# Performance work log

Hardware: AMD Instinct MI355X
Metric: run time of the kernel (lower is better)

Reference implementation:

```python
import jax, jax.numpy as jnp
import numpy as np
import math

B, L, D, H = 8, 2048, 1024, 1024


def setup_inputs() -> dict:
    key = jax.random.key(0)
    ks = jax.random.split(key, 6)
    scale = 1.0 / math.sqrt(D)
    return {
        "input_q": jax.random.normal(ks[0], (B, L, D), dtype=jnp.float32),
        "input_k": jax.random.normal(ks[1], (B, L, D), dtype=jnp.float32),
        "k_mask": jax.random.uniform(ks[2], (B, L), dtype=jnp.float32),
        "Wq": jax.random.normal(ks[3], (D, H), dtype=jnp.float32) * scale,
        "bq": jnp.zeros((H,), dtype=jnp.float32),
        "Wk": jax.random.normal(ks[4], (D, H), dtype=jnp.float32) * scale,
        "bk": jnp.zeros((H,), dtype=jnp.float32),
    }


def reference(input_q, input_k, k_mask, Wq, bq, Wk, bk):
    # Linear projections: (b, l, d) @ (d, h) -> (b, l, h)
    q = input_q @ Wq + bq
    k = input_k @ Wk + bk
    # Faithful to original: mask values become 0.0 or -1e9, then an
    # outer product bmm((b,l,1),(b,1,l)) builds the (b,l,l) additive mask.
    m = jnp.where(k_mask > 0.5, 0.0, -1000000000.0)  # (b, l)
    add_mask = m[:, :, None] * m[:, None, :]          # (b, l, l) outer product
    # Scaled dot-product scores
    attn = jnp.einsum("bqh,bkh->bqk", q, k) / math.sqrt(H)
    attn = jax.nn.softmax(attn + add_mask, axis=-1)
    # Weighted sum over the ORIGINAL input_k (not projected k), as in source
    out = jnp.einsum("bqk,bkd->bqd", attn, input_k)
    return out
```

## Files before the change

### kernel.cpp

```cpp
#include <hip/hip_runtime.h>

#define BATCH 8
#define SEQ   2048
#define DIM   1024

typedef __attribute__((ext_vector_type(8)))  short short8;
typedef __attribute__((ext_vector_type(4)))  short short4v;
typedef __attribute__((ext_vector_type(4)))  float floatx4;
typedef __attribute__((ext_vector_type(16))) float floatx16;

__device__ __forceinline__ unsigned short f32_to_bf16(float f) {
    union { float f; unsigned int u; } x; x.f = f;
    unsigned int r = x.u + 0x7fffu + ((x.u >> 16) & 1u);
    return (unsigned short)(r >> 16);
}

__device__ __forceinline__ float bf16_to_f32(unsigned short h) {
    union { unsigned int u; float f; } x; x.u = ((unsigned int)h) << 16;
    return x.f;
}

__device__ __forceinline__ void async_load16(const void* g, void* l) {
    __builtin_amdgcn_global_load_lds(
        (const __attribute__((address_space(1))) void*)g,
        (__attribute__((address_space(3))) void*)l, 16, 0, 0);
}

__global__ __launch_bounds__(256) void build_idx(
    const float* __restrict__ mask, int* __restrict__ idx,
    int* __restrict__ cnt, int* __restrict__ padcnt)
{
    const int b = blockIdx.x;
    const int t = threadIdx.x;
    const float* mb = mask + b * SEQ;
    int flags[8]; int c = 0;
#pragma unroll
    for (int j = 0; j < 8; ++j) {
        flags[j] = (mb[t * 8 + j] > 0.5f) ? 1 : 0;
        c += flags[j];
    }
    int sc = c;
    for (int o = 1; o < 64; o <<= 1) {
        int v = __shfl_up(sc, o);
        if ((t & 63) >= o) sc += v;
    }
    __shared__ int wtot[4];
    const int lane = t & 63, wave = t >> 6;
    if (lane == 63) wtot[wave] = sc;
    __syncthreads();
    int woff = 0;
    for (int w = 0; w < wave; ++w) woff += wtot[w];
    int p = woff + sc - c;
#pragma unroll
    for (int j = 0; j < 8; ++j)
        if (flags[j]) idx[b * SEQ + (p++)] = t * 8 + j;
    __syncthreads();
    const int total = wtot[0] + wtot[1] + wtot[2] + wtot[3];
    if (t == 0) { cnt[b] = total; padcnt[b] = (total + 127) & ~127; }
    for (int q = total + t; q < SEQ; q += 256) idx[b * SEQ + q] = 0;
}

__global__ __launch_bounds__(256) void gather_cvt_q(
    const float* __restrict__ xq, const int* __restrict__ idx,
    const int* __restrict__ padcnt, unsigned short* __restrict__ qc)
{
    const int b = blockIdx.y;
    const int rc = blockIdx.x;
    if (rc >= padcnt[b]) return;
    const int src = idx[b * SEQ + rc];
    const float* s = xq + ((long)b * SEQ + src) * DIM + threadIdx.x * 4;
    unsigned short* d = qc + ((long)b * SEQ + rc) * DIM + threadIdx.x * 4;
    floatx4 v = *(const floatx4*)s;
    short4v w;
#pragma unroll
    for (int j = 0; j < 4; ++j) w[j] = (short)f32_to_bf16(v[j]);
    *(short4v*)d = w;
}

__global__ __launch_bounds__(256) void prep_kv(
    const float* __restrict__ xk, const float* __restrict__ mask,
    unsigned short* __restrict__ kbf, unsigned short* __restrict__ Vt,
    float* __restrict__ mavg)
{
    __shared__ float tile[32][33];
    __shared__ float msk[32];
    __shared__ float csum[8][32];
    const int b  = blockIdx.z;
    const int c0 = blockIdx.x * 32;
    const int r0 = blockIdx.y * 32;
    const int tx = threadIdx.x & 31, ty = threadIdx.x >> 5;
    const float* xb = xk + (long)b * SEQ * DIM;
    unsigned short* kb = kbf + (long)b * SEQ * DIM;
    unsigned short* vb = Vt + (long)b * DIM * SEQ;

    if (threadIdx.x < 32) msk[threadIdx.x] = mask[b * SEQ + r0 + threadIdx.x];

    float v[4];
#pragma unroll
    for (int i = 0; i < 4; ++i) {
        const int r = ty + i * 8;
        v[i] = xb[(long)(r0 + r) * DIM + c0 + tx];
        tile[r][tx] = v[i];
        kb[(long)(r0 + r) * DIM + c0 + tx] = f32_to_bf16(v[i]);
    }
    __syncthreads();

    float s = 0.f;
#pragma unroll
    for (int i = 0; i < 4; ++i) {
        const int r = ty + i * 8;
        s += (msk[r] <= 0.5f) ? v[i] : 0.f;
    }
    csum[ty][tx] = s;

#pragma unroll
    for (int i = 0; i < 4; ++i) {
        const int c = ty + i * 8;
        vb[(long)(c0 + c) * SEQ + r0 + tx] = f32_to_bf16(tile[tx][c]);
    }
    __syncthreads();
    if (ty == 0) {
        float t = 0.f;
#pragma unroll
        for (int j = 0; j < 8; ++j) t += csum[j][tx];
        atomicAdd(&mavg[b * DIM + c0 + tx], t);
    }
}

__global__ __launch_bounds__(256) void cvt_bf16_2(
    const float* __restrict__ s0, unsigned short* __restrict__ d0,
    const float* __restrict__ s1, unsigned short* __restrict__ d1)
{
    const int hi = blockIdx.x >> 9;
    const float* src = hi ? s1 : s0;
    unsigned short* dst = hi ? d1 : d0;
    const long i = ((long)(blockIdx.x & 511) * 256 + threadIdx.x) * 8;
    floatx4 v0 = *(const floatx4*)(src + i);
    floatx4 v1 = *(const floatx4*)(src + i + 4);
    short8 w;
#pragma unroll
    for (int j = 0; j < 4; ++j) w[j]     = (short)f32_to_bf16(v0[j]);
#pragma unroll
    for (int j = 0; j < 4; ++j) w[4 + j] = (short)f32_to_bf16(v1[j]);
    *(short8*)(dst + i) = w;
}

__global__ __launch_bounds__(256) void proj_bias(
    const float* __restrict__ bq, const float* __restrict__ Wk, float* __restrict__ g0)
{
    const int n = blockIdx.x;
    const int t = threadIdx.x;
    float s = 0.f;
    for (int h = t; h < DIM; h += 256) s += bq[h] * Wk[(long)n * DIM + h];
    for (int o = 32; o; o >>= 1) s += __shfl_xor(s, o);
    __shared__ float r[4];
    if ((t & 63) == 0) r[t >> 6] = s;
    __syncthreads();
    if (t == 0) g0[n] = r[0] + r[1] + r[2] + r[3];
}

template<bool C_BF16, bool BIAS, bool LIMIT, bool SCATTER, int FLAT>
__global__ __launch_bounds__(256, 4) void gemm_bt(
    const unsigned short* __restrict__ A, const unsigned short* __restrict__ Bt,
    void* __restrict__ Cp, const float* __restrict__ bias,
    int N, int K, long sA, long sB, long sC, float scale,
    const int* __restrict__ mlim, const int* __restrict__ cntp,
    const int* __restrict__ idx, int sh)
{
    int bx, by, bz;
    if (FLAT == 0) {
        bx = blockIdx.x; by = blockIdx.y; bz = blockIdx.z;
    } else {
        const int id = blockIdx.x;
        bz = id & 7;
        const int rem = id >> 3;
        const int m = (1 << sh) - 1;
        if (FLAT == 1) { bx = rem & m; by = rem >> sh; }
        else           { by = rem & m; bx = rem >> sh; }
    }
    const int row0 = bx * 128;
    if (LIMIT && row0 >= mlim[bz]) return;

    __shared__ unsigned short As[128 * 64];
    __shared__ unsigned short Bs[128 * 64];

    const int tid  = threadIdx.x;
    const int lane = tid & 63;
    const int wave = tid >> 6;
    const int wm   = wave >> 1;
    const int wn   = wave & 1;
    const int l31  = lane & 31;
    const int half = lane >> 5;
    const int x7   = lane & 7;
    const int col0 = by * 128;

    const int sr = lane >> 3;
    const int sq = ((lane & 7) ^ sr) * 8;

    const long K8 = (long)K * 8;
    const unsigned short* aRow =
        A + (long)bz * sA + (long)row0 * K + (long)(wave * 32 + sr) * K + sq;
    const unsigned short* bRow =
        Bt + (long)bz * sB + (long)col0 * K + (long)(wave * 32 + sr) * K + sq;

    floatx16 acc[2][2];
#pragma unroll
    for (int a = 0; a < 2; ++a)
#pragma unroll
        for (int b = 0; b < 2; ++b)
#pragma unroll
            for (int r = 0; r < 16; ++r) acc[a][b][r] = 0.f;

    const int raf[2] = { (wm * 64 +  0 + l31) * 64, (wm * 64 + 32 + l31) * 64 };
    const int rbf[2] = { (wn * 64 +  0 + l31) * 64, (wn * 64 + 32 + l31) * 64 };

    for (int kt = 0; kt < K; kt += 64) {
#pragma unroll
        for (int c = 0; c < 4; ++c) {
            const int chunk = wave * 4 + c;
            async_load16(aRow + kt + c * K8, As + chunk * 512);
            async_load16(bRow + kt + c * K8, Bs + chunk * 512);
        }
        __syncthreads();

#pragma unroll
        for (int ks = 0; ks < 4; ++ks) {
            const int sw = ((ks * 2 + half) ^ x7) << 3;
            short8 af[2], bf[2];
#pragma unroll
            for (int t = 0; t < 2; ++t) {
                af[t] = *(const short8*)(As + raf[t] + sw);
                bf[t] = *(const short8*)(Bs + rbf[t] + sw);
            }
#pragma unroll
            for (int tm = 0; tm < 2; ++tm)
#pragma unroll
                for (int tn = 0; tn < 2; ++tn)
                    acc[tm][tn] = __builtin_amdgcn_mfma_f32_32x32x16_bf16(
                        af[tm], bf[tn], acc[tm][tn], 0, 0, 0);
        }
        __syncthreads();
    }

    const long zC = (long)bz * sC;
    const int climit = SCATTER ? cntp[bz] : 0;
    const int* ridx  = SCATTER ? (idx + bz * SEQ) : (const int*)nullptr;
#pragma unroll
    for (int tn = 0; tn < 2; ++tn) {
        const int ccol = col0 + wn * 64 + tn * 32 + l31;
        float bv = 0.f;
        if (BIAS) bv = bias[ccol];
#pragma unroll
        for (int tm = 0; tm < 2; ++tm) {
            const int rbase = row0 + wm * 64 + tm * 32 + 4 * half;
#pragma unroll
            for (int r = 0; r < 16; ++r) {
                const int crow = rbase + (r & 3) + 8 * (r >> 2);
                float v = acc[tm][tn][r] * scale + bv;
                long orow = crow;
                if (SCATTER) {
                    if (crow >= climit) continue;
                    orow = ridx[crow];
                }
                const long ci = zC + orow * (long)N + ccol;
                if (C_BF16) ((unsigned short*)Cp)[ci] = f32_to_bf16(v);
                else        ((float*)Cp)[ci] = v;
            }
        }
    }
}

__global__ __launch_bounds__(256) void softmax_rows(
    unsigned short* __restrict__ S, const int* __restrict__ padcnt)
{
    const int b = blockIdx.x >> 11, rc = blockIdx.x & 2047;
    if (rc >= padcnt[b]) return;
    const long base = (long)blockIdx.x * SEQ + threadIdx.x * 8;
    const int lane = threadIdx.x & 63, wave = threadIdx.x >> 6;
    __shared__ float rbuf[8];

    short8 v = *(const short8*)(S + base);
    float x[8];
#pragma unroll
    for (int j = 0; j < 8; ++j) x[j] = bf16_to_f32((unsigned short)v[j]);

    float m = x[0];
#pragma unroll
    for (int j = 1; j < 8; ++j) m = fmaxf(m, x[j]);
    for (int o = 32; o; o >>= 1) m = fmaxf(m, __shfl_xor(m, o));
    if (lane == 0) rbuf[wave] = m;
    __syncthreads();
    m = fmaxf(fmaxf(rbuf[0], rbuf[1]), fmaxf(rbuf[2], rbuf[3]));

    float e[8], s = 0.f;
#pragma unroll
    for (int j = 0; j < 8; ++j) { e[j] = __expf(x[j] - m); s += e[j]; }
    for (int o = 32; o; o >>= 1) s += __shfl_xor(s, o);
    if (lane == 0) rbuf[4 + wave] = s;
    __syncthreads();
    s = rbuf[4] + rbuf[5] + rbuf[6] + rbuf[7];
    const float inv = 1.0f / s;

    short8 o8;
#pragma unroll
    for (int j = 0; j < 8; ++j) o8[j] = (short)f32_to_bf16(e[j] * inv);
    *(short8*)(S + base) = o8;
}

__global__ __launch_bounds__(256) void overwrite_masked(
    float* __restrict__ out, const float* __restrict__ mask,
    const float* __restrict__ mavg, const int* __restrict__ cnt)
{
    const int bid = blockIdx.x;
    const int b = bid >> 11;
    if (mask[bid] > 0.5f) return;
    const float inv = 1.0f / (float)(SEQ - cnt[b]);
    const long obase = (long)bid * DIM;
    const float* mv = mavg + b * DIM;
    for (int d = threadIdx.x; d < DIM; d += 256)
        out[obase + d] = mv[d] * inv;
}

extern "C" void kernel_launch(void* const* d_in, const int* in_sizes, int n_in,
                              void* d_out, int out_size, void* d_ws, size_t ws_size,
                              hipStream_t stream) {
    (void)in_sizes; (void)n_in; (void)out_size;
    const float* input_q = (const float*)d_in[0];
    const float* input_k = (const float*)d_in[1];
    const float* k_mask  = (const float*)d_in[2];
    const float* Wq      = (const float*)d_in[3];
    const float* bq      = (const float*)d_in[4];
    const float* Wk      = (const float*)d_in[5];
    const float* bk      = (const float*)d_in[6];
    (void)bk;
    float* out = (float*)d_out;

    char* ws = (char*)d_ws;
    unsigned short* qc   = (unsigned short*)(ws);
    unsigned short* S    = (unsigned short*)(ws);
    unsigned short* qpp  = (unsigned short*)(ws + 67108864);
    unsigned short* Wqb  = (unsigned short*)(ws + 67108864);
    unsigned short* Wkb  = (unsigned short*)(ws + 69206016);
    unsigned short* kbf  = (unsigned short*)(ws + 100663296);
    unsigned short* Vt   = (unsigned short*)(ws + 134217728);
    unsigned short* Gt   = (unsigned short*)(ws + 167772160);
    float*          g0   = (float*)(ws + 169869312);
    float*          mavg = (float*)(ws + 169873408);
    int*            idx  = (int*)(ws + 169906176);
    int*            cnts = (int*)(ws + 169971712);
    int*            pcnt = (int*)(ws + 169971744);
    if (ws_size < 169971776) return;

    hipMemsetAsync(mavg, 0, BATCH * DIM * sizeof(float), stream);

    build_idx<<<BATCH, 256, 0, stream>>>(k_mask, idx, cnts, pcnt);
    gather_cvt_q<<<dim3(SEQ, BATCH), 256, 0, stream>>>(input_q, idx, pcnt, qc);
    prep_kv<<<dim3(DIM / 32, SEQ / 32, BATCH), 256, 0, stream>>>(input_k, k_mask, kbf, Vt, mavg);
    cvt_bf16_2<<<1024, 256, 0, stream>>>(Wq, Wqb, Wk, Wkb);
    proj_bias<<<DIM, 256, 0, stream>>>(bq, Wk, g0);

    gemm_bt<true, false, false, false, 0><<<dim3(8, 8, 1), 256, 0, stream>>>(
        Wkb, Wqb, Gt, nullptr, DIM, DIM, 0, 0, 0, 1.0f, nullptr, nullptr, nullptr, 0);

    gemm_bt<true, true, true, false, 2><<<8 * 16 * 8, 256, 0, stream>>>(
        qc, Gt, qpp, g0, DIM, DIM,
        (long)SEQ * DIM, 0, (long)SEQ * DIM, 1.0f, pcnt, nullptr, nullptr, 3);

    gemm_bt<true, false, true, false, 1><<<8 * 16 * 16, 256, 0, stream>>>(
        qpp, kbf, S, nullptr, SEQ, DIM,
        (long)SEQ * DIM, (long)SEQ * DIM, (long)SEQ * SEQ, 0.03125f, pcnt, nullptr, nullptr, 4);

    softmax_rows<<<BATCH * SEQ, 256, 0, stream>>>(S, pcnt);

    gemm_bt<false, false, true, true, 2><<<8 * 16 * 8, 256, 0, stream>>>(
        S, Vt, out, nullptr, DIM, SEQ,
        (long)SEQ * SEQ, (long)DIM * SEQ, (long)SEQ * DIM, 1.0f, pcnt, cnts, idx, 3);

    overwrite_masked<<<BATCH * SEQ, 256, 0, stream>>>(out, k_mask, mavg, cnts);
}
```

Before: 371.0 us.

## Merge small prep kernels and fold masked-row fill into final GEMM launch

Combines the mask index build, the mavg zeroing, the Wq/Wk bf16 conversion and the bias projection into one prep_misc launch, replacing a memset and four separate launches. The final S·V GEMM launch gets extra blocks that write the masked-row mean output, so the separate overwrite_masked kernel goes away. prep_kv now works on 64x64 tiles with vectorized float4 loads and 4-wide bf16 stores. The aim is fewer launch gaps and better memory efficiency in the transpose, at the cost of a larger LDS tile and branchy fused kernels.

```diff
diff --git a/kernel.cpp b/kernel.cpp
--- a/kernel.cpp
+++ b/kernel.cpp
@@ -26,38 +26,68 @@
         (__attribute__((address_space(3))) void*)l, 16, 0, 0);
 }
 
-__global__ __launch_bounds__(256) void build_idx(
+__global__ __launch_bounds__(256) void prep_misc(
     const float* __restrict__ mask, int* __restrict__ idx,
-    int* __restrict__ cnt, int* __restrict__ padcnt)
+    int* __restrict__ cnt, int* __restrict__ padcnt, float* __restrict__ mavg,
+    const float* __restrict__ Wq, unsigned short* __restrict__ Wqb,
+    const float* __restrict__ Wk, unsigned short* __restrict__ Wkb,
+    const float* __restrict__ bq, float* __restrict__ g0)
 {
-    const int b = blockIdx.x;
-    const int t = threadIdx.x;
-    const float* mb = mask + b * SEQ;
-    int flags[8]; int c = 0;
-#pragma unroll
-    for (int j = 0; j < 8; ++j) {
-        flags[j] = (mb[t * 8 + j] > 0.5f) ? 1 : 0;
-        c += flags[j];
-    }
-    int sc = c;
-    for (int o = 1; o < 64; o <<= 1) {
-        int v = __shfl_up(sc, o);
-        if ((t & 63) >= o) sc += v;
-    }
     __shared__ int wtot[4];
-    const int lane = t & 63, wave = t >> 6;
-    if (lane == 63) wtot[wave] = sc;
-    __syncthreads();
-    int woff = 0;
-    for (int w = 0; w < wave; ++w) woff += wtot[w];
-    int p = woff + sc - c;
-#pragma unroll
-    for (int j = 0; j < 8; ++j)
-        if (flags[j]) idx[b * SEQ + (p++)] = t * 8 + j;
-    __syncthreads();
-    const int total = wtot[0] + wtot[1] + wtot[2] + wtot[3];
-    if (t == 0) { cnt[b] = total; padcnt[b] = (total + 127) & ~127; }
-    for (int q = total + t; q < SEQ; q += 256) idx[b * SEQ + q] = 0;
+    __shared__ float rshared[4];
+    const int id = blockIdx.x;
+    const int t  = threadIdx.x;
+
+    if (id < 8) {
+        const int b = id;
+        for (int d = t; d < DIM; d += 256) mavg[b * DIM + d] = 0.f;
+        const float* mb = mask + b * SEQ;
+        int flags[8]; int c = 0;
+#pragma unroll
+        for (int j = 0; j < 8; ++j) {
+            flags[j] = (mb[t * 8 + j] > 0.5f) ? 1 : 0;
+            c += flags[j];
+        }
+        int sc = c;
+        for (int o = 1; o < 64; o <<= 1) {
+            int v = __shfl_up(sc, o);
+            if ((t & 63) >= o) sc += v;
+        }
+        const int lane = t & 63, wave = t >> 6;
+        if (lane == 63) wtot[wave] = sc;
+        __syncthreads();
+        int woff = 0;
+        for (int w = 0; w < wave; ++w) woff += wtot[w];
+        int p = woff + sc - c;
+#pragma unroll
+        for (int j = 0; j < 8; ++j)
+            if (flags[j]) idx[b * SEQ + (p++)] = t * 8 + j;
+        __syncthreads();
+        const int total = wtot[0] + wtot[1] + wtot[2] + wtot[3];
+        if (t == 0) { cnt[b] = total; padcnt[b] = (total + 127) & ~127; }
+        for (int q = total + t; q < SEQ; q += 256) idx[b * SEQ + q] = 0;
+    } else if (id < 1032) {
+        const int k = id - 8;
+        const float* src = (k < 512) ? Wq : Wk;
+        unsigned short* dst = (k < 512) ? Wqb : Wkb;
+        const long i = ((long)(k & 511) * 256 + t) * 8;
+        floatx4 v0 = *(const floatx4*)(src + i);
+        floatx4 v1 = *(const floatx4*)(src + i + 4);
+        short8 w;
+#pragma unroll
+        for (int j = 0; j < 4; ++j) w[j]     = (short)f32_to_bf16(v0[j]);
+#pragma unroll
+        for (int j = 0; j < 4; ++j) w[4 + j] = (short)f32_to_bf16(v1[j]);
+        *(short8*)(dst + i) = w;
+    } else {
+        const int n = id - 1032;
+        float s = 0.f;
+        for (int h = t; h < DIM; h += 256) s += bq[h] * Wk[(long)n * DIM + h];
+        for (int o = 32; o; o >>= 1) s += __shfl_xor(s, o);
+        if ((t & 63) == 0) rshared[t >> 6] = s;
+        __syncthreads();
+        if (t == 0) g0[n] = rshared[0] + rshared[1] + rshared[2] + rshared[3];
+    }
 }
 
 __global__ __launch_bounds__(256) void gather_cvt_q(
@@ -82,91 +112,97 @@
     unsigned short* __restrict__ kbf, unsigned short* __restrict__ Vt,
     float* __restrict__ mavg)
 {
-    __shared__ float tile[32][33];
-    __shared__ float msk[32];
-    __shared__ float csum[8][32];
+    __shared__ float tile[64][65];
+    __shared__ float msk[64];
+    __shared__ float csum[4][64];
     const int b  = blockIdx.z;
-    const int c0 = blockIdx.x * 32;
-    const int r0 = blockIdx.y * 32;
-    const int tx = threadIdx.x & 31, ty = threadIdx.x >> 5;
+    const int c0 = blockIdx.x * 64;
+    const int r0 = blockIdx.y * 64;
+    const int cg = threadIdx.x & 15;
+    const int rr = threadIdx.x >> 4;
     const float* xb = xk + (long)b * SEQ * DIM;
     unsigned short* kb = kbf + (long)b * SEQ * DIM;
     unsigned short* vb = Vt + (long)b * DIM * SEQ;
 
-    if (threadIdx.x < 32) msk[threadIdx.x] = mask[b * SEQ + r0 + threadIdx.x];
-
-    float v[4];
+    if (threadIdx.x < 64) msk[threadIdx.x] = mask[b * SEQ + r0 + threadIdx.x];
+
 #pragma unroll
     for (int i = 0; i < 4; ++i) {
-        const int r = ty + i * 8;
-        v[i] = xb[(long)(r0 + r) * DIM + c0 + tx];
-        tile[r][tx] = v[i];
-        kb[(long)(r0 + r) * DIM + c0 + tx] = f32_to_bf16(v[i]);
+        const int row = rr + i * 16;
+        const floatx4 v = *(const floatx4*)(xb + (long)(r0 + row) * DIM + c0 + cg * 4);
+        short4v w;
+#pragma unroll
+        for (int j = 0; j < 4; ++j) {
+            tile[row][cg * 4 + j] = v[j];
+            w[j] = (short)f32_to_bf16(v[j]);
+        }
+        *(short4v*)(kb + (long)(r0 + row) * DIM + c0 + cg * 4) = w;
     }
     __syncthreads();
 
-    float s = 0.f;
-#pragma unroll
-    for (int i = 0; i < 4; ++i) {
-        const int r = ty + i * 8;
-        s += (msk[r] <= 0.5f) ? v[i] : 0.f;
-    }
-    csum[ty][tx] = s;
-
-#pragma unroll
-    for (int i = 0; i < 4; ++i) {
-        const int c = ty + i * 8;
-        vb[(long)(c0 + c) * SEQ + r0 + tx] = f32_to_bf16(tile[tx][c]);
+    {
+        const int rgroup = threadIdx.x >> 6;
+        const int c = threadIdx.x & 63;
+        float s = 0.f;
+#pragma unroll
+        for (int r = 0; r < 16; ++r) {
+            const int row = rgroup * 16 + r;
+            s += (msk[row] <= 0.5f) ? tile[row][c] : 0.f;
+        }
+        csum[rgroup][c] = s;
+    }
+
+    {
+        const int sg = threadIdx.x & 15;
+        const int ch = threadIdx.x >> 4;
+#pragma unroll
+        for (int i = 0; i < 4; ++i) {
+            const int c = ch + i * 16;
+            short4v w;
+#pragma unroll
+            for (int j = 0; j < 4; ++j) w[j] = (short)f32_to_bf16(tile[sg * 4 + j][c]);
+            *(short4v*)(vb + (long)(c0 + c) * SEQ + r0 + sg * 4) = w;
+        }
     }
     __syncthreads();
-    if (ty == 0) {
-        float t = 0.f;
-#pragma unroll
-        for (int j = 0; j < 8; ++j) t += csum[j][tx];
-        atomicAdd(&mavg[b * DIM + c0 + tx], t);
-    }
-}
-
-__global__ __launch_bounds__(256) void cvt_bf16_2(
-    const float* __restrict__ s0, unsigned short* __restrict__ d0,
-    const float* __restrict__ s1, unsigned short* __restrict__ d1)
-{
-    const int hi = blockIdx.x >> 9;
-    const float* src = hi ? s1 : s0;
-    unsigned short* dst = hi ? d1 : d0;
-    const long i = ((long)(blockIdx.x & 511) * 256 + threadIdx.x) * 8;
-    floatx4 v0 = *(const floatx4*)(src + i);
-    floatx4 v1 = *(const floatx4*)(src + i + 4);
-    short8 w;
-#pragma unroll
-    for (int j = 0; j < 4; ++j) w[j]     = (short)f32_to_bf16(v0[j]);
-#pragma unroll
-    for (int j = 0; j < 4; ++j) w[4 + j] = (short)f32_to_bf16(v1[j]);
-    *(short8*)(dst + i) = w;
-}
-
-__global__ __launch_bounds__(256) void proj_bias(
-    const float* __restrict__ bq, const float* __restrict__ Wk, float* __restrict__ g0)
-{
-    const int n = blockIdx.x;
-    const int t = threadIdx.x;
-    float s = 0.f;
-    for (int h = t; h < DIM; h += 256) s += bq[h] * Wk[(long)n * DIM + h];
-    for (int o = 32; o; o >>= 1) s += __shfl_xor(s, o);
-    __shared__ float r[4];
-    if ((t & 63) == 0) r[t >> 6] = s;
-    __syncthreads();
-    if (t == 0) g0[n] = r[0] + r[1] + r[2] + r[3];
-}
-
-template<bool C_BF16, bool BIAS, bool LIMIT, bool SCATTER, int FLAT>
+    if (threadIdx.x < 64) {
+        const int c = threadIdx.x;
+        const float tot = csum[0][c] + csum[1][c] + csum[2][c] + csum[3][c];
+        atomicAdd(&mavg[b * DIM + c0 + c], tot);
+    }
+}
+
+template<bool C_BF16, bool BIAS, bool LIMIT, bool SCATTER, int FLAT, bool MFILL>
 __global__ __launch_bounds__(256, 4) void gemm_bt(
     const unsigned short* __restrict__ A, const unsigned short* __restrict__ Bt,
     void* __restrict__ Cp, const float* __restrict__ bias,
     int N, int K, long sA, long sB, long sC, float scale,
     const int* __restrict__ mlim, const int* __restrict__ cntp,
-    const int* __restrict__ idx, int sh)
+    const int* __restrict__ idx, int sh,
+    const float* __restrict__ kmask, const float* __restrict__ fmavg)
 {
+    if (MFILL && blockIdx.x >= 1024) {
+        const int id2 = blockIdx.x - 1024;
+        const int b = id2 >> 8;
+        const int row = ((id2 & 255) << 3) + (threadIdx.x >> 5);
+        if (kmask[b * SEQ + row] <= 0.5f) {
+            const float inv = 1.0f / (float)(SEQ - cntp[b]);
+            float* ob = (float*)Cp + ((long)b * SEQ + row) * DIM;
+            const float* mv = fmavg + b * DIM;
+            const int l32 = threadIdx.x & 31;
+#pragma unroll
+            for (int i = 0; i < 8; ++i) {
+                const int d = (l32 + i * 32) * 4;
+                const floatx4 s = *(const floatx4*)(mv + d);
+                floatx4 o;
+#pragma unroll
+                for (int j = 0; j < 4; ++j) o[j] = s[j] * inv;
+                *(floatx4*)(ob + d) = o;
+            }
+        }
+        return;
+    }
+
     int bx, by, bz;
     if (FLAT == 0) {
         bx = blockIdx.x; by = blockIdx.y; bz = blockIdx.z;
@@ -305,20 +341,6 @@
 #pragma unroll
     for (int j = 0; j < 8; ++j) o8[j] = (short)f32_to_bf16(e[j] * inv);
     *(short8*)(S + base) = o8;
-}
-
-__global__ __launch_bounds__(256) void overwrite_masked(
-    float* __restrict__ out, const float* __restrict__ mask,
-    const float* __restrict__ mavg, const int* __restrict__ cnt)
-{
-    const int bid = blockIdx.x;
-    const int b = bid >> 11;
-    if (mask[bid] > 0.5f) return;
-    const float inv = 1.0f / (float)(SEQ - cnt[b]);
-    const long obase = (long)bid * DIM;
-    const float* mv = mavg + b * DIM;
-    for (int d = threadIdx.x; d < DIM; d += 256)
-        out[obase + d] = mv[d] * inv;
 }
 
 extern "C" void kernel_launch(void* const* d_in, const int* in_sizes, int n_in,
@@ -351,30 +373,29 @@
     int*            pcnt = (int*)(ws + 169971744);
     if (ws_size < 169971776) return;
 
-    hipMemsetAsync(mavg, 0, BATCH * DIM * sizeof(float), stream);
-
-    build_idx<<<BATCH, 256, 0, stream>>>(k_mask, idx, cnts, pcnt);
+    prep_misc<<<2056, 256, 0, stream>>>(k_mask, idx, cnts, pcnt, mavg,
+                                        Wq, Wqb, Wk, Wkb, bq, g0);
     gather_cvt_q<<<dim3(SEQ, BATCH), 256, 0, stream>>>(input_q, idx, pcnt, qc);
-    prep_kv<<<dim3(DIM / 32, SEQ / 32, BATCH), 256, 0, stream>>>(input_k, k_mask, kbf, Vt, mavg);
-    cvt_bf16_2<<<1024, 256, 0, stream>>>(Wq, Wqb, Wk, Wkb);
-    proj_bias<<<DIM, 256, 0, stream>>>(bq, Wk, g0);
-
-    gemm_bt<true, false, false, false, 0><<<dim3(8, 8, 1), 256, 0, stream>>>(
-        Wkb, Wqb, Gt, nullptr, DIM, DIM, 0, 0, 0, 1.0f, nullptr, nullptr, nullptr, 0);
-
-    gemm_bt<true, true, true, false, 2><<<8 * 16 * 8, 256, 0, stream>>>(
+    prep_kv<<<dim3(DIM / 64, SEQ / 64, BATCH), 256, 0, stream>>>(input_k, k_mask, kbf, Vt, mavg);
+
+    gemm_bt<true, false, false, false, 0, false><<<dim3(8, 8, 1), 256, 0, stream>>>(
+        Wkb, Wqb, Gt, nullptr, DIM, DIM, 0, 0, 0, 1.0f,
+        nullptr, nullptr, nullptr, 0, nullptr, nullptr);
+
+    gemm_bt<true, true, true, false, 2, false><<<8 * 16 * 8, 256, 0, stream>>>(
         qc, Gt, qpp, g0, DIM, DIM,
-        (long)SEQ * DIM, 0, (long)SEQ * DIM, 1.0f, pcnt, nullptr, nullptr, 3);
-
-    gemm_bt<true, false, true, false, 1><<<8 * 16 * 16, 256, 0, stream>>>(
+        (long)SEQ * DIM, 0, (long)SEQ * DIM, 1.0f,
+        pcnt, nullptr, nullptr, 3, nullptr, nullptr);
+
+    gemm_bt<true, false, true, false, 1, false><<<8 * 16 * 16, 256, 0, stream>>>(
         qpp, kbf, S, nullptr, SEQ, DIM,
-        (long)SEQ * DIM, (long)SEQ * DIM, (long)SEQ * SEQ, 0.03125f, pcnt, nullptr, nullptr, 4);
+        (long)SEQ * DIM, (long)SEQ * DIM, (long)SEQ * SEQ, 0.03125f,
+        pcnt, nullptr, nullptr, 4, nullptr, nullptr);
 
     softmax_rows<<<BATCH * SEQ, 256, 0, stream>>>(S, pcnt);
 
-    gemm_bt<false, false, true, true, 2><<<8 * 16 * 8, 256, 0, stream>>>(
+    gemm_bt<false, false, true, true, 2, true><<<1024 + 2048, 256, 0, stream>>>(
         S, Vt, out, nullptr, DIM, SEQ,
-        (long)SEQ * SEQ, (long)DIM * SEQ, (long)SEQ * DIM, 1.0f, pcnt, cnts, idx, 3);
-
-    overwrite_masked<<<BATCH * SEQ, 256, 0, stream>>>(out, k_mask, mavg, cnts);
-}
+        (long)SEQ * SEQ, (long)DIM * SEQ, (long)SEQ * DIM, 1.0f,
+        pcnt, cnts, idx, 3, k_mask, mavg);
+}
```

Result: faster. 349.6 us (-5.8%).
